# Optimization experiments

Measured on AMD Instinct MI355X. Metric: run time of the kernel, lower is better.

Reference implementation:

```python
import jax, jax.numpy as jnp
import numpy as np

B, D, H, W = 512, 32, 128, 128


def setup_inputs() -> dict:
    key = jax.random.key(0)
    k1, k2, k3, k4 = jax.random.split(key, 4)
    inputs = jax.random.uniform(k1, (B, D), dtype=jnp.float32)
    stamp = jax.random.uniform(k2, (H, W, 1), dtype=jnp.float32)
    rows = jax.random.randint(k3, (D,), 0, H)
    cols = jax.random.randint(k4, (D,), 0, W)
    coords = jnp.stack([rows, cols], axis=-1).astype(jnp.int32)  # [D,2]
    return {"inputs": inputs, "stamp": stamp, "coords": coords}


def _static_indices(d, h, w):
    # rows/cols replication counts (static, numpy)
    rows_per = np.full(d, h // d, np.int32); rows_per[: h % d] += 1
    cols_per = np.full(d, w // d, np.int32); cols_per[: w % d] += 1
    # equidistant bar layout
    bar_w = w // (3 * d + 2)
    total_gap = w - d * bar_w
    gap = total_gap // (d + 1)
    extra = total_gap - gap * (d + 1)
    beg = extra // 2
    col_to_bar = np.full(w, -1, np.int32)
    for i in range(d):
        s = beg + i * (bar_w + gap) + gap
        col_to_bar[s : s + bar_w] = i
    return rows_per, cols_per, col_to_bar


def reference(inputs, stamp, coords):
    b, d = inputs.shape
    h, w = stamp.shape[:2]
    rows_per, cols_per, col_to_bar = _static_indices(d, h, w)

    # channel 1: deepinsight scatter (duplicates sum, matching tf.scatter_nd)
    di = jnp.zeros((b, h, w), inputs.dtype).at[:, coords[:, 0], coords[:, 1]].add(inputs)

    # channel 2: row-wise copy
    row_idx = np.repeat(np.arange(d), rows_per)  # [h]
    rowcopy = jnp.broadcast_to(inputs[:, row_idx][:, :, None], (b, h, w))

    # channel 3: normalized pairwise abs distance, expanded to h x w
    dm = jnp.abs(inputs[:, :, None] - inputs[:, None, :])  # [b,d,d]
    mn = jnp.min(dm, axis=(1, 2), keepdims=True)
    mx = jnp.max(dm, axis=(1, 2), keepdims=True)
    nd = (dm - mn) / (mx - mn)
    nd = nd[:, np.repeat(np.arange(d), rows_per), :][:, :, np.repeat(np.arange(d), cols_per)]

    # channel 4: equidistant bar graph (bars fill rows [0, bar_height))
    bar_height = jnp.clip(jnp.round(inputs * h).astype(jnp.int32), 0, h)  # [b,d]
    mask = (jnp.arange(h)[None, :, None] < bar_height[:, None, :]).astype(inputs.dtype)  # [b,h,d]
    safe = np.where(col_to_bar < 0, 0, col_to_bar)
    bars = mask[:, :, safe] * (col_to_bar >= 0).astype(inputs.dtype)[None, None, :]  # [b,h,w]

    stamp_b = jnp.broadcast_to(stamp, (b, h, w, 1))
    return jnp.concatenate(
        [stamp_b, di[..., None], rowcopy[..., None], nd[..., None], bars[..., None]], axis=-1
    )
```

## Files before the change

### kernel.cpp

```cpp
#include <hip/hip_runtime.h>


__global__ __launch_bounds__(256) void di_main(const float* __restrict__ inputs,
                                               const float* __restrict__ stamp,
                                               float* __restrict__ out) {
    const int blk = blockIdx.x;
    const int b = blk >> 4;
    const int part = blk & 15;
    const int tid = threadIdx.x;

    __shared__ float xs[32];
    __shared__ int bh[32];
    __shared__ float buf[256 * 20];

    if (tid < 32) {
        float v = inputs[b * 32 + tid];
        xs[tid] = v;
        int t = (int)rintf(v * 128.0f);
        bh[tid] = t < 0 ? 0 : (t > 128 ? 128 : t);
    }
    __syncthreads();

    float mn = xs[0], mx = xs[0];
#pragma unroll
    for (int d = 1; d < 32; ++d) {
        float v = xs[d];
        mn = fminf(mn, v);
        mx = fmaxf(mx, v);
    }
    const float inv = 1.0f / (mx - mn);

    const int lp = part * 1024 + tid * 4;
    const int h = lp >> 7;
    const int w0 = lp & 127;

    const float rowv = xs[h >> 2];
    const float ndv = fabsf(rowv - xs[w0 >> 2]) * inv;

    const float4 sv = *reinterpret_cast<const float4*>(stamp + h * 128 + w0);
    const float svj[4] = {sv.x, sv.y, sv.z, sv.w};

    alignas(16) float vals[20];
#pragma unroll
    for (int j = 0; j < 4; ++j) {
        const int w = w0 + j;
        float barv = 0.0f;
        const int t = w - 17;
        if (t >= 0 && t <= 93 && (t % 3) == 0) {
            const int bar = t / 3;
            barv = (h < bh[bar]) ? 1.0f : 0.0f;
        }
        vals[5 * j + 0] = svj[j];
        vals[5 * j + 1] = 0.0f;
        vals[5 * j + 2] = rowv;
        vals[5 * j + 3] = ndv;
        vals[5 * j + 4] = barv;
    }

    float4* lw = reinterpret_cast<float4*>(&buf[tid * 20]);
    const float4* src = reinterpret_cast<const float4*>(vals);
#pragma unroll
    for (int k = 0; k < 5; ++k) lw[k] = src[k];
    __syncthreads();

    float4* dst = reinterpret_cast<float4*>(out + ((size_t)b * 16384 + (size_t)part * 1024) * 5);
    const float4* lr = reinterpret_cast<const float4*>(buf);
#pragma unroll
    for (int it = 0; it < 5; ++it) {
        const int f = it * 256 + tid;
        dst[f] = lr[f];
    }
}

__global__ __launch_bounds__(256) void di_scatter(const float* __restrict__ inputs,
                                                  const int* __restrict__ coords,
                                                  float* __restrict__ out) {
    const int i = blockIdx.x * blockDim.x + threadIdx.x;
    if (i >= 512 * 32) return;
    const int b = i >> 5;
    const int d = i & 31;
    const int r = coords[2 * d], c = coords[2 * d + 1];
    atomicAdd(&out[(((size_t)b * 128 + r) * 128 + c) * 5 + 1], inputs[i]);
}

extern "C" void kernel_launch(void* const* d_in, const int* in_sizes, int n_in,
                              void* d_out, int out_size, void* d_ws, size_t ws_size,
                              hipStream_t stream) {
    const float* inputs = (const float*)d_in[0];
    const float* stamp  = (const float*)d_in[1];
    const int*   coords = (const int*)d_in[2];
    float* out = (float*)d_out;

    di_main<<<8192, 256, 0, stream>>>(inputs, stamp, out);
    di_scatter<<<64, 256, 0, stream>>>(inputs, coords, out);
}
```

Baseline: 169.6 us.

## Fuse scatter into main kernel via shared-memory atomics and shuffle min/max

The separate scatter kernel is removed. Each block now adds the scattered inputs that fall into its 8-row slice directly into the shared staging buffer before the coalesced store. This drops a second kernel launch and its global atomics on already-written output. The per-thread 32-element serial min/max is also replaced by a wavefront shuffle reduction broadcast through shared memory, at the cost of one extra barrier per block.

New measurement: 167.7 us. No clear change (-1.1%).

```diff
diff --git a/kernel.cpp b/kernel.cpp
--- a/kernel.cpp
+++ b/kernel.cpp
@@ -3,6 +3,7 @@
 
 __global__ __launch_bounds__(256) void di_main(const float* __restrict__ inputs,
                                                const float* __restrict__ stamp,
+                                               const int* __restrict__ coords,
                                                float* __restrict__ out) {
     const int blk = blockIdx.x;
     const int b = blk >> 4;
@@ -11,24 +12,27 @@
 
     __shared__ float xs[32];
     __shared__ int bh[32];
+    __shared__ float sinv;
     __shared__ float buf[256 * 20];
 
-    if (tid < 32) {
-        float v = inputs[b * 32 + tid];
-        xs[tid] = v;
-        int t = (int)rintf(v * 128.0f);
-        bh[tid] = t < 0 ? 0 : (t > 128 ? 128 : t);
+    if (tid < 64) {
+        float v = inputs[b * 32 + (tid & 31)];
+        if (tid < 32) {
+            xs[tid] = v;
+            int t = (int)rintf(v * 128.0f);
+            bh[tid] = t < 0 ? 0 : (t > 128 ? 128 : t);
+        }
+        float mn = v, mx = v;
+#pragma unroll
+        for (int off = 1; off < 32; off <<= 1) {
+            mn = fminf(mn, __shfl_xor(mn, off));
+            mx = fmaxf(mx, __shfl_xor(mx, off));
+        }
+        if (tid == 0) sinv = 1.0f / (mx - mn);
     }
     __syncthreads();
 
-    float mn = xs[0], mx = xs[0];
-#pragma unroll
-    for (int d = 1; d < 32; ++d) {
-        float v = xs[d];
-        mn = fminf(mn, v);
-        mx = fmaxf(mx, v);
-    }
-    const float inv = 1.0f / (mx - mn);
+    const float inv = sinv;
 
     const int lp = part * 1024 + tid * 4;
     const int h = lp >> 7;
@@ -63,6 +67,13 @@
     for (int k = 0; k < 5; ++k) lw[k] = src[k];
     __syncthreads();
 
+    if (tid < 32) {
+        const int r = coords[2 * tid], c = coords[2 * tid + 1];
+        if ((r >> 3) == part)
+            atomicAdd(&buf[((r & 7) * 128 + c) * 5 + 1], xs[tid]);
+    }
+    __syncthreads();
+
     float4* dst = reinterpret_cast<float4*>(out + ((size_t)b * 16384 + (size_t)part * 1024) * 5);
     const float4* lr = reinterpret_cast<const float4*>(buf);
 #pragma unroll
@@ -70,17 +81,6 @@
         const int f = it * 256 + tid;
         dst[f] = lr[f];
     }
-}
-
-__global__ __launch_bounds__(256) void di_scatter(const float* __restrict__ inputs,
-                                                  const int* __restrict__ coords,
-                                                  float* __restrict__ out) {
-    const int i = blockIdx.x * blockDim.x + threadIdx.x;
-    if (i >= 512 * 32) return;
-    const int b = i >> 5;
-    const int d = i & 31;
-    const int r = coords[2 * d], c = coords[2 * d + 1];
-    atomicAdd(&out[(((size_t)b * 128 + r) * 128 + c) * 5 + 1], inputs[i]);
 }
 
 extern "C" void kernel_launch(void* const* d_in, const int* in_sizes, int n_in,
@@ -91,6 +91,5 @@
     const int*   coords = (const int*)d_in[2];
     float* out = (float*)d_out;
 
-    di_main<<<8192, 256, 0, stream>>>(inputs, stamp, out);
-    di_scatter<<<64, 256, 0, stream>>>(inputs, coords, out);
+    di_main<<<8192, 256, 0, stream>>>(inputs, stamp, coords, out);
 }
```
